# Performance work log

Hardware: AMD Instinct MI355X
Metric: run time of the kernel (lower is better)

Reference implementation:

```python
import jax, jax.numpy as jnp
import numpy as np

DIST_THRESHOLD = 900.0  # distance_threshold from __init__
NO_CODE_ID = -1         # no_code_id from __init__


def setup_inputs() -> dict:
    key = jax.random.key(0)
    k1, k2 = jax.random.split(key)
    x = jax.random.normal(k1, (4, 2048, 512), dtype=jnp.float32)      # [b, n, d] tokens
    codes = jax.random.normal(k2, (16384, 512), dtype=jnp.float32)    # [c, d] full codebook
    return {"x": x, "codes": codes}


def reference(x, codes):
    x2 = jnp.sum(x * x, axis=-1, keepdims=True)            # [b, n, 1]
    c2 = jnp.sum(codes * codes, axis=-1)                   # [c]
    xc = jnp.einsum('bnd,cd->bnc', x, codes)               # [b, n, c] (the compute-heavy GEMM)
    dist_sq = jnp.maximum(x2 + c2 - 2.0 * xc, 0.0)         # clamp tiny negatives, like cdist

    within = jnp.any(dist_sq <= DIST_THRESHOLD, axis=-1)   # [b, n]
    nn_ids = jnp.argmin(dist_sq, axis=-1)                  # [b, n]
    ids = jnp.where(within, nn_ids, NO_CODE_ID)            # tokens outside threshold -> no_code_id
    return ids
```

## Files before the change

kernel.cpp:

```cpp
#include <hip/hip_runtime.h>


#define NTOK   8192
#define NCODES 16384
#define DDIM   512
#define NCHUNK 8
#define CHUNK  2048
#define DIST_THR 900.0f

typedef unsigned short u16;
typedef _Float16 half8 __attribute__((ext_vector_type(8)));
typedef float    f32x4 __attribute__((ext_vector_type(4)));

__device__ __forceinline__ void conv_body(const float* __restrict__ src,
                                          u16* __restrict__ dh,
                                          u16* __restrict__ dl, int c) {
    int r = c & 15, q = (c >> 4) & 3, g = (c >> 6) & 7, kit = (c >> 9) & 15;
    int tile = c >> 13;
    int row = tile * 128 + g * 16 + r;
    int k = kit * 32 + q * 8;
    const float* p = src + (size_t)row * DDIM + k;
    float4 v0 = *(const float4*)p;
    float4 v1 = *(const float4*)(p + 4);
    float vv[8] = {v0.x, v0.y, v0.z, v0.w, v1.x, v1.y, v1.z, v1.w};
    u16 hs[8], ls[8];
    #pragma unroll
    for (int j = 0; j < 8; ++j) {
        float sv = vv[j] * 16.0f;
        _Float16 h = (_Float16)sv;
        float hf = (float)h;
        _Float16 l = (_Float16)(sv - hf);
        union { _Float16 f; u16 u; } uh, ul;
        uh.f = h; ul.f = l;
        hs[j] = uh.u; ls[j] = ul.u;
    }
    uint4 H, L;
    H.x = hs[0] | ((unsigned)hs[1] << 16); H.y = hs[2] | ((unsigned)hs[3] << 16);
    H.z = hs[4] | ((unsigned)hs[5] << 16); H.w = hs[6] | ((unsigned)hs[7] << 16);
    L.x = ls[0] | ((unsigned)ls[1] << 16); L.y = ls[2] | ((unsigned)ls[3] << 16);
    L.z = ls[4] | ((unsigned)ls[5] << 16); L.w = ls[6] | ((unsigned)ls[7] << 16);
    *(uint4*)(dh + (size_t)c * 8) = H;
    *(uint4*)(dl + (size_t)c * 8) = L;
}

__global__ __launch_bounds__(256) void nn_prep(const float* __restrict__ x,
                                               const float* __restrict__ codes,
                                               u16* __restrict__ xh, u16* __restrict__ xl,
                                               u16* __restrict__ ch, u16* __restrict__ cl,
                                               float* __restrict__ c2) {
    int b = blockIdx.x;
    if (b < 2048) {
        conv_body(x, xh, xl, b * 256 + threadIdx.x);
    } else if (b < 6144) {
        conv_body(codes, ch, cl, (b - 2048) * 256 + threadIdx.x);
    } else {
        int w = threadIdx.x >> 6;
        int lane = threadIdx.x & 63;
        int c = (b - 6144) * 4 + w;
        const float* p = codes + (size_t)c * DDIM + lane * 8;
        float4 v0 = *(const float4*)p;
        float4 v1 = *(const float4*)(p + 4);
        float s = v0.x*v0.x + v0.y*v0.y + v0.z*v0.z + v0.w*v0.w
                + v1.x*v1.x + v1.y*v1.y + v1.z*v1.z + v1.w*v1.w;
        #pragma unroll
        for (int off = 32; off > 0; off >>= 1) s += __shfl_down(s, off);
        if (lane == 0) c2[c] = s;
    }
}

__global__ __launch_bounds__(512, 2) void nn_gemm(const u16* __restrict__ xh,
                                                  const u16* __restrict__ xl,
                                                  const u16* __restrict__ chh,
                                                  const u16* __restrict__ cll,
                                                  const float* __restrict__ c2,
                                                  float* __restrict__ pmin,
                                                  int* __restrict__ pid) {
    __shared__ __align__(16) char smem[131072];
    const int tid = threadIdx.x;
    const int lane = tid & 63;
    const int wave = tid >> 6;
    const int wm = wave & 3;
    const int wn = wave >> 2;
    const int mtile = blockIdx.x >> 3;
    const int chunk = blockIdx.x & 7;
    const int m0 = mtile * 256;

    const int plane = wave >> 1;
    const int tsub  = wave & 1;
    const bool isA = (plane < 2);
    const u16* gbase;
    if (plane == 0)      gbase = xh  + ((size_t)(mtile * 2 + tsub) * 16) * 4096;
    else if (plane == 1) gbase = xl  + ((size_t)(mtile * 2 + tsub) * 16) * 4096;
    else if (plane == 2) gbase = chh + ((size_t)(chunk * 16 + tsub) * 16) * 4096;
    else                 gbase = cll + ((size_t)(chunk * 16 + tsub) * 16) * 4096;
    gbase += lane * 8;
    const int ldsoff = wave * 8192;

    float mv[16];
    int   mi[16];
    #pragma unroll
    for (int s = 0; s < 16; ++s) { mv[s] = 3.4e38f; mi[s] = 0; }

    f32x4 acc[4][8];
    #pragma unroll
    for (int i = 0; i < 4; ++i)
        #pragma unroll
        for (int j = 0; j < 8; ++j) acc[i][j] = (f32x4)0.0f;

    auto stage = [&](int it2) {
        int kit2 = it2 & 15, nt2 = it2 >> 4;
        size_t off = (size_t)(isA ? kit2 : nt2 * 32 + kit2) * 4096;
        const u16* src = gbase + off;
        char* dst = smem + (size_t)(it2 & 1) * 65536 + ldsoff;
        #pragma unroll
        for (int s = 0; s < 8; ++s)
            __builtin_amdgcn_global_load_lds(
                (const __attribute__((address_space(1))) void*)(src + s * 512),
                (__attribute__((address_space(3))) void*)(dst + s * 1024),
                16, 0, 0);
    };

    stage(0);
    for (int it = 0; it < 128; ++it) {
        __syncthreads();

        const char* cur = smem + (size_t)(it & 1) * 65536;
        half8 ah[4], al[4], bh[8], bl[8];
        #pragma unroll
        for (int i = 0; i < 4; ++i) {
            int g = wm * 4 + i;
            ah[i] = *(const half8*)(cur +         g * 1024 + lane * 16);
            al[i] = *(const half8*)(cur + 16384 + g * 1024 + lane * 16);
        }
        #pragma unroll
        for (int j = 0; j < 8; ++j) {
            int g = wn * 8 + j;
            bh[j] = *(const half8*)(cur + 32768 + g * 1024 + lane * 16);
            bl[j] = *(const half8*)(cur + 49152 + g * 1024 + lane * 16);
        }

        __builtin_amdgcn_sched_barrier(0);

        if (it < 127) stage(it + 1);

        #pragma unroll
        for (int j = 0; j < 8; ++j)
            #pragma unroll
            for (int i = 0; i < 4; ++i) {
                acc[i][j] = __builtin_amdgcn_mfma_f32_16x16x32_f16(ah[i], bh[j], acc[i][j], 0, 0, 0);
                acc[i][j] = __builtin_amdgcn_mfma_f32_16x16x32_f16(ah[i], bl[j], acc[i][j], 0, 0, 0);
                acc[i][j] = __builtin_amdgcn_mfma_f32_16x16x32_f16(al[i], bh[j], acc[i][j], 0, 0, 0);
            }

        if ((it & 15) == 15) {
            int nt = it >> 4;
            #pragma unroll
            for (int j = 0; j < 8; ++j) {
                int ncol = nt * 256 + wn * 128 + j * 16 + (lane & 15);
                int gid = chunk * CHUNK + ncol;
                float cv = c2[gid];
                #pragma unroll
                for (int i = 0; i < 4; ++i)
                    #pragma unroll
                    for (int r = 0; r < 4; ++r) {
                        float s = fmaf(acc[i][j][r], -0.0078125f, cv);
                        int slot = i * 4 + r;
                        if (s < mv[slot]) { mv[slot] = s; mi[slot] = gid; }
                    }
            }
            #pragma unroll
            for (int i = 0; i < 4; ++i)
                #pragma unroll
                for (int j = 0; j < 8; ++j) acc[i][j] = (f32x4)0.0f;
        }
    }

    #pragma unroll
    for (int off = 1; off < 16; off <<= 1) {
        #pragma unroll
        for (int s = 0; s < 16; ++s) {
            float ov = __shfl_xor(mv[s], off);
            int   oi = __shfl_xor(mi[s], off);
            if (ov < mv[s] || (ov == mv[s] && oi < mi[s])) { mv[s] = ov; mi[s] = oi; }
        }
    }
    if ((lane & 15) == 0) {
        #pragma unroll
        for (int i = 0; i < 4; ++i)
            #pragma unroll
            for (int r = 0; r < 4; ++r) {
                int row = wm * 64 + i * 16 + (lane >> 4) * 4 + r;
                int2 e;
                e.x = __float_as_int(mv[i * 4 + r]);
                e.y = mi[i * 4 + r];
                *(int2*)(smem + (wn * 256 + row) * 8) = e;
            }
    }
    __syncthreads();
    if (tid < 256) {
        int2 e0 = *(const int2*)(smem + tid * 8);
        int2 e1 = *(const int2*)(smem + (256 + tid) * 8);
        float v0 = __int_as_float(e0.x), v1 = __int_as_float(e1.x);
        float bv = v0; int bi = e0.y;
        if (v1 < bv || (v1 == bv && e1.y < bi)) { bv = v1; bi = e1.y; }
        pmin[(size_t)(m0 + tid) * NCHUNK + chunk] = bv;
        pid [(size_t)(m0 + tid) * NCHUNK + chunk] = bi;
    }
}

__global__ __launch_bounds__(256) void nn_fin(const float* __restrict__ x,
                                              const float* __restrict__ pmin,
                                              const int* __restrict__ pid,
                                              int* __restrict__ out) {
    int w = threadIdx.x >> 6;
    int lane = threadIdx.x & 63;
    int t = blockIdx.x * 4 + w;
    const float* p = x + (size_t)t * DDIM + lane * 8;
    float4 v0 = *(const float4*)p;
    float4 v1 = *(const float4*)(p + 4);
    float s = v0.x*v0.x + v0.y*v0.y + v0.z*v0.z + v0.w*v0.w
            + v1.x*v1.x + v1.y*v1.y + v1.z*v1.z + v1.w*v1.w;
    #pragma unroll
    for (int off = 32; off > 0; off >>= 1) s += __shfl_down(s, off);
    if (lane == 0) {
        const float* pm = pmin + (size_t)t * NCHUNK;
        const int*   pi = pid  + (size_t)t * NCHUNK;
        float bv = pm[0]; int bi = pi[0];
        #pragma unroll
        for (int c = 1; c < NCHUNK; ++c) {
            float v = pm[c]; int id = pi[c];
            if (v < bv || (v == bv && id < bi)) { bv = v; bi = id; }
        }
        float mind = s + bv;
        out[t] = (mind <= DIST_THR) ? bi : -1;
    }
}

extern "C" void kernel_launch(void* const* d_in, const int* in_sizes, int n_in,
                              void* d_out, int out_size, void* d_ws, size_t ws_size,
                              hipStream_t stream) {
    const float* x     = (const float*)d_in[0];
    const float* codes = (const float*)d_in[1];
    int* out = (int*)d_out;

    char* ws = (char*)d_ws;
    u16*   xh   = (u16*)(ws);
    u16*   xl   = (u16*)(ws + 8388608);
    u16*   chh  = (u16*)(ws + 16777216);
    u16*   cll  = (u16*)(ws + 33554432);
    float* c2   = (float*)(ws + 50331648);
    float* pmin = (float*)(ws + 50397184);
    int*   pid  = (int*)  (ws + 50659328);

    nn_prep<<<10240, 256, 0, stream>>>(x, codes, xh, xl, chh, cll, c2);
    nn_gemm<<<32 * NCHUNK, 512, 0, stream>>>(xh, xl, chh, cll, c2, pmin, pid);
    nn_fin<<<NTOK / 4, 256, 0, stream>>>(x, pmin, pid, out);
}
```

Measured before the change: 418.9 us.

## Load A fragments directly from global memory, stage only codebook tiles in LDS

The A operand (x hi/lo planes) is now read by each wave straight from global memory into registers every k-step, and no longer staged through LDS. Only the codebook B tiles go through LDS, which halves shared memory to 64KB per block and halves the global-to-LDS staging per iteration. The goal is to cut LDS traffic and footprint, which may allow higher occupancy. The cost is that the direct global A loads are issued right before the MFMAs without being prefetched, so their latency can stall compute, and A tiles are re-read from global/L2 for every n-tile.

```diff
diff --git a/kernel.cpp b/kernel.cpp
--- a/kernel.cpp
+++ b/kernel.cpp
@@ -75,7 +75,7 @@
                                                   const float* __restrict__ c2,
                                                   float* __restrict__ pmin,
                                                   int* __restrict__ pid) {
-    __shared__ __align__(16) char smem[131072];
+    __shared__ __align__(16) char smem[65536];
     const int tid = threadIdx.x;
     const int lane = tid & 63;
     const int wave = tid >> 6;
@@ -85,16 +85,10 @@
     const int chunk = blockIdx.x & 7;
     const int m0 = mtile * 256;
 
-    const int plane = wave >> 1;
-    const int tsub  = wave & 1;
-    const bool isA = (plane < 2);
-    const u16* gbase;
-    if (plane == 0)      gbase = xh  + ((size_t)(mtile * 2 + tsub) * 16) * 4096;
-    else if (plane == 1) gbase = xl  + ((size_t)(mtile * 2 + tsub) * 16) * 4096;
-    else if (plane == 2) gbase = chh + ((size_t)(chunk * 16 + tsub) * 16) * 4096;
-    else                 gbase = cll + ((size_t)(chunk * 16 + tsub) * 16) * 4096;
-    gbase += lane * 8;
-    const int ldsoff = wave * 8192;
+    size_t aoff = ((size_t)(mtile * 2 + (wm >> 1)) * 16) * 8192
+                + (size_t)((wm & 1) * 4) * 1024 + (size_t)lane * 16;
+    const char* Ahb = (const char*)xh + aoff;
+    const char* Alb = (const char*)xl + aoff;
 
     float mv[16];
     int   mi[16];
@@ -109,38 +103,44 @@
 
     auto stage = [&](int it2) {
         int kit2 = it2 & 15, nt2 = it2 >> 4;
-        size_t off = (size_t)(isA ? kit2 : nt2 * 32 + kit2) * 4096;
-        const u16* src = gbase + off;
-        char* dst = smem + (size_t)(it2 & 1) * 65536 + ldsoff;
-        #pragma unroll
-        for (int s = 0; s < 8; ++s)
+        char* dstbuf = smem + (size_t)(it2 & 1) * 32768;
+        #pragma unroll
+        for (int s = 0; s < 4; ++s) {
+            int seg = wave * 4 + s;
+            const u16* base = (seg < 16) ? chh : cll;
+            int sub = (seg >> 3) & 1;
+            int part = seg & 7;
+            const u16* src = base
+                + ((size_t)((chunk * 16 + nt2 * 2 + sub) * 16 + kit2)) * 4096
+                + part * 512 + lane * 8;
             __builtin_amdgcn_global_load_lds(
-                (const __attribute__((address_space(1))) void*)(src + s * 512),
-                (__attribute__((address_space(3))) void*)(dst + s * 1024),
+                (const __attribute__((address_space(1))) void*)src,
+                (__attribute__((address_space(3))) void*)(dstbuf + seg * 1024),
                 16, 0, 0);
+        }
     };
 
     stage(0);
     for (int it = 0; it < 128; ++it) {
         __syncthreads();
 
-        const char* cur = smem + (size_t)(it & 1) * 65536;
-        half8 ah[4], al[4], bh[8], bl[8];
+        int kit = it & 15;
+        half8 ah[4], al[4];
         #pragma unroll
         for (int i = 0; i < 4; ++i) {
-            int g = wm * 4 + i;
-            ah[i] = *(const half8*)(cur +         g * 1024 + lane * 16);
-            al[i] = *(const half8*)(cur + 16384 + g * 1024 + lane * 16);
-        }
+            ah[i] = *(const half8*)(Ahb + (size_t)kit * 8192 + i * 1024);
+            al[i] = *(const half8*)(Alb + (size_t)kit * 8192 + i * 1024);
+        }
+        const char* cur = smem + (size_t)(it & 1) * 32768;
+        half8 bh[8], bl[8];
         #pragma unroll
         for (int j = 0; j < 8; ++j) {
             int g = wn * 8 + j;
-            bh[j] = *(const half8*)(cur + 32768 + g * 1024 + lane * 16);
-            bl[j] = *(const half8*)(cur + 49152 + g * 1024 + lane * 16);
+            bh[j] = *(const half8*)(cur +         g * 1024 + lane * 16);
+            bl[j] = *(const half8*)(cur + 16384 + g * 1024 + lane * 16);
         }
 
         __builtin_amdgcn_sched_barrier(0);
-
         if (it < 127) stage(it + 1);
 
         #pragma unroll
```

After: 536.4 us. +28.0%, slower.

## Replace direct global-to-LDS loads with register-staged prefetch interleaved with MFMA halves

Applied to the files above, without the earlier changes.

Replaces the global_load_lds async copies with explicit global loads into registers, written to the alternate LDS buffer after each half of the MFMA work. The B-fragment loads and MFMA loop are split into two halves, with odd/even waves processing the halves in swapped order to spread LDS bank traffic. The intent is finer interleaving of memory and matrix work and less register pressure from B fragments. In exchange it adds VGPR use for the staged data and extra LDS write instructions, which may hurt occupancy at launch bounds of 512 threads and 2 blocks.

```diff
diff --git a/kernel.cpp b/kernel.cpp
--- a/kernel.cpp
+++ b/kernel.cpp
@@ -81,6 +81,7 @@
     const int wave = tid >> 6;
     const int wm = wave & 3;
     const int wn = wave >> 2;
+    const int odd = wn;
     const int mtile = blockIdx.x >> 3;
     const int chunk = blockIdx.x & 7;
     const int m0 = mtile * 256;
@@ -107,50 +108,67 @@
         #pragma unroll
         for (int j = 0; j < 8; ++j) acc[i][j] = (f32x4)0.0f;
 
-    auto stage = [&](int it2) {
+    auto gsrc = [&](int it2, int s) -> const u16* {
         int kit2 = it2 & 15, nt2 = it2 >> 4;
         size_t off = (size_t)(isA ? kit2 : nt2 * 32 + kit2) * 4096;
-        const u16* src = gbase + off;
-        char* dst = smem + (size_t)(it2 & 1) * 65536 + ldsoff;
+        return gbase + off + s * 512;
+    };
+
+    {
+        uint4 g0[8];
+        #pragma unroll
+        for (int s = 0; s < 8; ++s) g0[s] = *(const uint4*)gsrc(0, s);
         #pragma unroll
         for (int s = 0; s < 8; ++s)
-            __builtin_amdgcn_global_load_lds(
-                (const __attribute__((address_space(1))) void*)(src + s * 512),
-                (__attribute__((address_space(3))) void*)(dst + s * 1024),
-                16, 0, 0);
-    };
-
-    stage(0);
+            *(uint4*)(smem + ldsoff + s * 1024 + lane * 16) = g0[s];
+    }
+
     for (int it = 0; it < 128; ++it) {
         __syncthreads();
 
         const char* cur = smem + (size_t)(it & 1) * 65536;
-        half8 ah[4], al[4], bh[8], bl[8];
+        char* nxt = smem + (size_t)(~it & 1) * 65536 + ldsoff;
+        const bool more = (it < 127);
+
+        half8 ah[4], al[4];
         #pragma unroll
         for (int i = 0; i < 4; ++i) {
             int g = wm * 4 + i;
             ah[i] = *(const half8*)(cur +         g * 1024 + lane * 16);
             al[i] = *(const half8*)(cur + 16384 + g * 1024 + lane * 16);
         }
-        #pragma unroll
-        for (int j = 0; j < 8; ++j) {
-            int g = wn * 8 + j;
-            bh[j] = *(const half8*)(cur + 32768 + g * 1024 + lane * 16);
-            bl[j] = *(const half8*)(cur + 49152 + g * 1024 + lane * 16);
-        }
-
-        __builtin_amdgcn_sched_barrier(0);
-
-        if (it < 127) stage(it + 1);
-
-        #pragma unroll
-        for (int j = 0; j < 8; ++j)
-            #pragma unroll
-            for (int i = 0; i < 4; ++i) {
-                acc[i][j] = __builtin_amdgcn_mfma_f32_16x16x32_f16(ah[i], bh[j], acc[i][j], 0, 0, 0);
-                acc[i][j] = __builtin_amdgcn_mfma_f32_16x16x32_f16(ah[i], bl[j], acc[i][j], 0, 0, 0);
-                acc[i][j] = __builtin_amdgcn_mfma_f32_16x16x32_f16(al[i], bh[j], acc[i][j], 0, 0, 0);
-            }
+
+        #pragma unroll
+        for (int h = 0; h < 2; ++h) {
+            const int jo = (h ^ odd) ? 4 : 0;
+            half8 bh[4], bl[4];
+            #pragma unroll
+            for (int jj = 0; jj < 4; ++jj) {
+                int g = wn * 8 + jo + jj;
+                bh[jj] = *(const half8*)(cur + 32768 + g * 1024 + lane * 16);
+                bl[jj] = *(const half8*)(cur + 49152 + g * 1024 + lane * 16);
+            }
+            uint4 gq[4];
+            if (more) {
+                #pragma unroll
+                for (int s = 0; s < 4; ++s) gq[s] = *(const uint4*)gsrc(it + 1, h * 4 + s);
+            }
+            #pragma unroll
+            for (int jj = 0; jj < 4; ++jj) {
+                int j = jo + jj;
+                #pragma unroll
+                for (int i = 0; i < 4; ++i) {
+                    acc[i][j] = __builtin_amdgcn_mfma_f32_16x16x32_f16(ah[i], bh[jj], acc[i][j], 0, 0, 0);
+                    acc[i][j] = __builtin_amdgcn_mfma_f32_16x16x32_f16(ah[i], bl[jj], acc[i][j], 0, 0, 0);
+                    acc[i][j] = __builtin_amdgcn_mfma_f32_16x16x32_f16(al[i], bh[jj], acc[i][j], 0, 0, 0);
+                }
+            }
+            if (more) {
+                #pragma unroll
+                for (int s = 0; s < 4; ++s)
+                    *(uint4*)(nxt + (h * 4 + s) * 1024 + lane * 16) = gq[s];
+            }
+        }
 
         if ((it & 15) == 15) {
             int nt = it >> 4;
```

Measured after the change: 684.4 us. +63.4%, slower.
